# Optimization experiments

Hardware: AMD Instinct MI355X
Metric: run time of the kernel (lower is better)

The kernel has to match this reference:

```python
import jax, jax.numpy as jnp
import numpy as np

EPS = 1e-5  # InstanceNorm2d default


def setup_inputs() -> dict:
    key = jax.random.key(0)
    ks = jax.random.split(key, 8)
    B, L, D, Q, C, H, W = 16, 24, 256, 256, 256, 128, 128
    s = 0.05
    return {
        "w_source": jax.random.normal(ks[0], (B, L, D), jnp.float32),
        "w_target": jax.random.normal(ks[1], (B, L, D), jnp.float32),
        "h": jax.random.normal(ks[2], (B, C, H, W), jnp.float32),
        "conv0_w": jax.random.normal(ks[3], (Q, C), jnp.float32) * s,   # 1x1 conv kernel
        "conv0_b": jnp.zeros((Q,), jnp.float32),
        "fck_w": jax.random.normal(ks[4], (Q, D), jnp.float32) * s,
        "fck_b": jnp.zeros((Q,), jnp.float32),
        "fc_w": jax.random.normal(ks[5], (2 * C, D), jnp.float32) * s,
        "fc_b": jnp.zeros((2 * C,), jnp.float32),
        "in_w": jnp.ones((C,), jnp.float32),
        "in_b": jnp.zeros((C,), jnp.float32),
    }


def reference(w_source, w_target, h, conv0_w, conv0_b, fck_w, fck_b, fc_w, fc_b, in_w, in_b):
    # ---- CrossAttention ----
    # q: 1x1 conv over h  -> [B,H,W,Q]
    q = jnp.einsum("bchw,qc->bhwq", h, conv0_w) + conv0_b
    # k: word keys        -> [B,L,Q]
    k = jnp.einsum("bld,qd->blq", w_source, fck_w) + fck_b
    attn = jnp.einsum("bhwq,blq->bhwl", q, k)  # [B,H,W,L]

    # ---- MaskingAllocation ----
    scores = jnp.einsum("bld,bmd->blm", w_source, w_target)       # [B,L,L]
    left = jnp.sum(scores, axis=1, keepdims=True) - scores        # [B,L,L]
    idx = jnp.argmax(left, axis=-1)                               # [B,L]
    w_alloc = jnp.take_along_axis(w_target, idx[..., None], axis=1)  # [B,L,D]

    # ---- modulation params ----
    bg = jnp.einsum("bld,ed->ble", w_alloc, fc_w) + fc_b          # [B,L,2C]
    beta, gamma = jnp.split(bg, 2, axis=-1)                       # each [B,L,C]
    beta_map = jnp.einsum("bhwl,blc->bchw", attn, beta)           # [B,C,H,W]
    gamma_map = jnp.einsum("bhwl,blc->bchw", attn, gamma)

    # ---- InstanceNorm2d (affine) + modulation ----
    mean = jnp.mean(h, axis=(2, 3), keepdims=True)
    var = jnp.var(h, axis=(2, 3), keepdims=True)
    hn = (h - mean) * jax.lax.rsqrt(var + EPS)
    hn = hn * in_w[None, :, None, None] + in_b[None, :, None, None]
    return hn * gamma_map + beta_map
```

## Files before the change

### kernel.cpp

```cpp
#include <hip/hip_runtime.h>
#include <stdint.h>

#define HW 16384
#define Bn 16
#define Ln 24
#define Dn 256
#define Qn 256
#define Cn 256

typedef __attribute__((ext_vector_type(8))) short short8;
typedef __attribute__((ext_vector_type(4))) float f32x4;

__device__ __forceinline__ unsigned short f2bf(float f) {
  unsigned u = __builtin_bit_cast(unsigned, f);
  u += 0x7FFFu + ((u >> 16) & 1u);
  return (unsigned short)(u >> 16);
}
__device__ __forceinline__ float bf2f(unsigned short s) {
  return __builtin_bit_cast(float, (unsigned)s << 16);
}

__device__ __forceinline__ void gl_lds16(const void* gsrc, void* lds) {
  __builtin_amdgcn_global_load_lds(
      (const __attribute__((address_space(1))) unsigned int*)gsrc,
      (__attribute__((address_space(3))) unsigned int*)lds, 16, 0, 0);
}

__global__ void k_keys(const float* __restrict__ wsrc, const float* __restrict__ fckw,
                       const float* __restrict__ fckb, float* __restrict__ kmat) {
  int b = blockIdx.x / Ln, l = blockIdx.x % Ln;
  __shared__ float row[Dn];
  row[threadIdx.x] = wsrc[(b * Ln + l) * Dn + threadIdx.x];
  __syncthreads();
  int q = threadIdx.x;
  const float* wq = fckw + q * Dn;
  float acc = fckb[q];
#pragma unroll 8
  for (int d = 0; d < Dn; ++d) acc += row[d] * wq[d];
  kmat[(b * Ln + l) * Qn + q] = acc;
}

__global__ void k_alloc(const float* __restrict__ wsrc, const float* __restrict__ wtgt,
                        const float* __restrict__ conv0b, const float* __restrict__ kmat,
                        float* __restrict__ walloc, float* __restrict__ bias0) {
  int b = blockIdx.x;
  __shared__ float S[Ln][Dn];
  __shared__ float T[Ln][Dn];
  __shared__ double sc[Ln][Ln];
  __shared__ double cs[Ln];
  __shared__ int idx[Ln];
  int tid = threadIdx.x;
  for (int n = tid; n < Ln * Dn; n += 256) {
    S[n >> 8][n & 255] = wsrc[b * Ln * Dn + n];
    T[n >> 8][n & 255] = wtgt[b * Ln * Dn + n];
  }
  __syncthreads();
  for (int p = tid; p < Ln * Ln; p += 256) {
    int l = p / Ln, m = p % Ln;
    double a = 0.0;
    for (int d = 0; d < Dn; ++d) a += (double)S[l][d] * (double)T[m][d];
    sc[l][m] = a;
  }
  __syncthreads();
  if (tid < Ln) {
    double a = 0.0;
    for (int l = 0; l < Ln; ++l) a += sc[l][tid];
    cs[tid] = a;
  }
  __syncthreads();
  if (tid < Ln) {
    double best = -1e300; int bi = 0;
    for (int m = 0; m < Ln; ++m) {
      double v = cs[m] - sc[tid][m];
      if (v > best) { best = v; bi = m; }
    }
    idx[tid] = bi;
  }
  __syncthreads();
  for (int n = tid; n < Ln * Dn; n += 256) {
    int l = n >> 8, d = n & 255;
    walloc[b * Ln * Dn + n] = T[idx[l]][d];
  }
  if (tid < Ln) {
    float a = 0.f;
    const float* kr = kmat + (b * Ln + tid) * Qn;
    for (int q = 0; q < Qn; ++q) a += conv0b[q] * kr[q];
    bias0[b * Ln + tid] = a;
  }
}

__global__ void k_mbg(const float* __restrict__ kmat, const float* __restrict__ conv0w,
                      const float* __restrict__ walloc, const float* __restrict__ fcw,
                      const float* __restrict__ fcb,
                      float* __restrict__ Mmat, float* __restrict__ bg) {
  int bid = blockIdx.x;
  __shared__ float row[Dn];
  if (bid < Bn * Ln) {
    int b = bid / Ln, l = bid % Ln;
    row[threadIdx.x] = kmat[(b * Ln + l) * Qn + threadIdx.x];
    __syncthreads();
    int c = threadIdx.x;
    float acc = 0.f;
    for (int q = 0; q < Qn; ++q) acc += row[q] * conv0w[q * Cn + c];
    Mmat[(b * Ln + l) * Cn + c] = acc;
  } else {
    int id = bid - Bn * Ln;
    int b = id / Ln, l = id % Ln;
    row[threadIdx.x] = walloc[(b * Ln + l) * Dn + threadIdx.x];
    __syncthreads();
    for (int it = 0; it < 2; ++it) {
      int e = it * 256 + threadIdx.x;
      const float* we = fcw + e * Dn;
      float acc = fcb[e];
      for (int d = 0; d < Dn; ++d) acc += row[d] * we[d];
      bg[(b * Ln + l) * (2 * Cn) + e] = acc;
    }
  }
}

__global__ void k_gbuild(const float* __restrict__ Mmat, const float* __restrict__ bg,
                         const float* __restrict__ bias0,
                         unsigned short* __restrict__ Gt, float* __restrict__ bv) {
  int g = blockIdx.x, b = blockIdx.y;
  __shared__ float Ms[Ln][Dn];
  __shared__ float Gb[Ln][128];
  __shared__ float B0[Ln];
  int tid = threadIdx.x;
  for (int n = tid; n < Ln * Dn; n += 256) Ms[n >> 8][n & 255] = Mmat[b * Ln * Dn + n];
  for (int n = tid; n < Ln * 128; n += 256) {
    int l = n >> 7, j = n & 127;
    int e = (j < 64) ? (Cn + g * 64 + j) : (g * 64 + (j - 64));
    Gb[l][j] = bg[(b * Ln + l) * (2 * Cn) + e];
  }
  if (tid < Ln) B0[tid] = bias0[b * Ln + tid];
  __syncthreads();
  char* base = (char*)Gt + (unsigned long)(b * 4 + g) * 65536;
  for (int r = 0; r < 128; ++r) {
    int isb = (r >> 4) & 1;
    int c_loc = (r >> 5) * 16 + (r & 15);
    int j = c_loc + isb * 64;
    float acc = 0.f;
#pragma unroll
    for (int l = 0; l < Ln; ++l) acc += Ms[l][tid] * Gb[l][j];
    unsigned off = (unsigned)((r * 512 + tid * 2) ^ ((r & 7) << 4));
    *(unsigned short*)(base + off) = f2bf(acc);
  }
  if (tid < 128) {
    float a = 0.f;
#pragma unroll
    for (int l = 0; l < Ln; ++l) a += B0[l] * Gb[l][tid];
    bv[b * 512 + g * 128 + tid] = a;
  }
}

__global__ void k_tr(const float* __restrict__ h, unsigned short* __restrict__ hT,
                     float* __restrict__ part) {
  int hwc = blockIdx.x;
  int cc  = blockIdx.y;
  int b   = blockIdx.z;
  int tid = threadIdx.x;
  int w = tid >> 6, lane = tid & 63;
  __shared__ unsigned short tile[64 * 258];
  __shared__ float red[64 * 17 + 16];
  const int c0 = cc * 64, hw0 = hwc * 256;
  for (int i = 0; i < 16; ++i) {
    int cl = i * 4 + w;
    f32x4 v = *(const f32x4*)(h + ((unsigned long)(b * Cn + c0 + cl)) * HW + hw0 + lane * 4);
    unsigned lo = (unsigned)f2bf(v.x) | ((unsigned)f2bf(v.y) << 16);
    unsigned hi = (unsigned)f2bf(v.z) | ((unsigned)f2bf(v.w) << 16);
    unsigned* dst = (unsigned*)(tile + cl * 258 + lane * 4);
    dst[0] = lo; dst[1] = hi;
  }
  __syncthreads();
  int cp = tid & 31, sub = tid >> 5;
  float s0 = 0.f, s20 = 0.f, s1 = 0.f, s21 = 0.f;
  for (int i = 0; i < 32; ++i) {
    int hw = i * 8 + sub;
    unsigned short a0 = tile[(2 * cp) * 258 + hw];
    unsigned short a1 = tile[(2 * cp + 1) * 258 + hw];
    float f0 = bf2f(a0), f1 = bf2f(a1);
    s0 += f0; s20 += f0 * f0; s1 += f1; s21 += f1 * f1;
    unsigned pk = (unsigned)a0 | ((unsigned)a1 << 16);
    *(unsigned*)(hT + ((unsigned long)b * HW + hw0 + hw) * Cn + c0 + 2 * cp) = pk;
  }
  red[(2 * cp) * 17 + sub * 2]     = s0;
  red[(2 * cp) * 17 + sub * 2 + 1] = s20;
  red[(2 * cp + 1) * 17 + sub * 2]     = s1;
  red[(2 * cp + 1) * 17 + sub * 2 + 1] = s21;
  __syncthreads();
  if (tid < 64) {
    float a = 0.f, q = 0.f;
#pragma unroll
    for (int j = 0; j < 8; ++j) { a += red[tid * 17 + j * 2]; q += red[tid * 17 + j * 2 + 1]; }
    float* pp = part + (((unsigned long)(b * Cn + c0 + tid)) * 64 + hwc) * 2;
    pp[0] = a; pp[1] = q;
  }
}

__global__ void k_fin(const float* __restrict__ part, const float* __restrict__ inw,
                      const float* __restrict__ inb, float* __restrict__ ss) {
  int id = blockIdx.x * 256 + threadIdx.x;
  int c = id & 255;
  float s = 0.f, s2 = 0.f;
  const float* pp = part + (unsigned long)id * 128;
  for (int j = 0; j < 64; ++j) { s += pp[2 * j]; s2 += pp[2 * j + 1]; }
  float mean = s * (1.0f / HW);
  float var = s2 * (1.0f / HW) - mean * mean;
  float rs = rsqrtf(var + 1e-5f);
  float scv = rs * inw[c];
  float sh = inb[c] - mean * scv;
  ss[id * 2] = scv; ss[id * 2 + 1] = sh;
}

__global__ __launch_bounds__(512, 1) void k_main(
    const unsigned short* __restrict__ hT, const unsigned short* __restrict__ Gt,
    const float* __restrict__ bv, const float* __restrict__ ss,
    float* __restrict__ out) {
  int x = blockIdx.x;
  int o = x & 7, idx = x >> 3;
  int b = idx >> 2, g = idx & 3;
  int tid = threadIdx.x;
  int w = tid >> 6, lane = tid & 63;
  int mw = w >> 2, nw = w & 3;
  int lr = lane & 15, lg = lane >> 4;

  __shared__ __align__(16) unsigned char Ab[65536];
  __shared__ __align__(16) unsigned char Bb[4][16384];

  const char* Gblob = (const char*)Gt + (unsigned long)(b * 4 + g) * 65536;
  const char* hTb = (const char*)hT + (unsigned long)b * HW * 512;

#pragma unroll
  for (int i = 0; i < 8; ++i)
    gl_lds16(Gblob + i * 8192 + w * 1024 + lane * 16, &Ab[i * 8192 + w * 1024]);

#define STAGE_B(c2, buf_)                                                        \
  {                                                                              \
    int s2_ = (c2) & 7, t2_ = (c2) >> 3;                                         \
    const char* base_ = hTb + (unsigned long)((o * 8 + t2_) * 256) * 512;        \
    _Pragma("unroll")                                                            \
    for (int l_ = 0; l_ < 2; ++l_) {                                             \
      int rowg_ = l_ * 128 + w * 16 + (lane >> 2);                               \
      int bir_ = s2_ * 64 + ((((lane & 3) << 4)) ^ (((rowg_ >> 1) & 3) << 4));   \
      gl_lds16(base_ + (unsigned long)rowg_ * 512 + bir_,                        \
               &Bb[buf_][l_ * 8192 + w * 1024]);                                 \
    }                                                                            \
  }

  f32x4 acc[4][4];
#pragma unroll
  for (int mf = 0; mf < 4; ++mf)
#pragma unroll
    for (int nf = 0; nf < 4; ++nf) acc[mf][nf] = (f32x4){0.f, 0.f, 0.f, 0.f};

  unsigned short h16[2][4][4];
  const float* ssb = ss + b * Cn * 2;
  const float* bvb = bv + b * 512 + g * 128;
  const int ssnap = 2 * g + mw;

  STAGE_B(0, 0);
  STAGE_B(1, 1);
  STAGE_B(2, 2);
  STAGE_B(3, 3);
  asm volatile("s_waitcnt vmcnt(6)" ::: "memory");
  __builtin_amdgcn_s_barrier();
  __builtin_amdgcn_sched_barrier(0);

#define COMPUTE(ch_, s_)                                                         \
  {                                                                              \
    const unsigned char* Bcur = &Bb[(ch_) & 3][0];                               \
    if ((s_) == ssnap) {                                                         \
      _Pragma("unroll") for (int p = 0; p < 2; ++p)                              \
      _Pragma("unroll") for (int nf = 0; nf < 4; ++nf) {                         \
        int row = nw * 64 + nf * 16 + lr;                                        \
        int sw = ((row >> 1) & 3) << 4;                                          \
        _Pragma("unroll") for (int r = 0; r < 4; ++r) {                          \
          int kloc = p * 16 + lg * 4 + r;                                        \
          h16[p][nf][r] = *(const unsigned short*)(&Bcur[row * 64 + ((kloc * 2) ^ sw)]); \
        }                                                                        \
      }                                                                          \
    }                                                                            \
    short8 afr[4], bfr[4];                                                       \
    _Pragma("unroll") for (int mf = 0; mf < 4; ++mf) {                           \
      int row = mw * 64 + mf * 16 + lr;                                          \
      afr[mf] = *(const short8*)(                                                \
          &Ab[row * 512 + (((s_) * 64 + lg * 16) ^ ((row & 7) << 4))]);          \
    }                                                                            \
    _Pragma("unroll") for (int nf = 0; nf < 4; ++nf) {                           \
      int row = nw * 64 + nf * 16 + lr;                                          \
      bfr[nf] = *(const short8*)(                                                \
          &Bcur[row * 64 + ((lg << 4) ^ (((row >> 1) & 3) << 4))]);              \
    }                                                                            \
    _Pragma("unroll") for (int mf = 0; mf < 4; ++mf)                             \
      _Pragma("unroll") for (int nf = 0; nf < 4; ++nf)                           \
        acc[mf][nf] = __builtin_amdgcn_mfma_f32_16x16x32_bf16(afr[mf], bfr[nf],  \
                                                              acc[mf][nf], 0, 0, 0); \
  }

#define EPILOGUE(t_)                                                             \
  {                                                                              \
    int hwbase = (o * 8 + (t_)) * 256 + nw * 64 + lr;                            \
    _Pragma("unroll") for (int p = 0; p < 2; ++p)                                \
    _Pragma("unroll") for (int r = 0; r < 4; ++r) {                              \
      int c_loc = (mw * 2 + p) * 16 + lg * 4 + r;                                \
      int cch = g * 64 + c_loc;                                                  \
      float scv = ssb[cch * 2], sh = ssb[cch * 2 + 1];                           \
      float bvg = bvb[c_loc], bvbt = bvb[64 + c_loc];                            \
      float* orow = out + (unsigned long)(b * Cn + cch) * HW + hwbase;           \
      _Pragma("unroll") for (int nf = 0; nf < 4; ++nf) {                         \
        float hn = bf2f(h16[p][nf][r]) * scv + sh;                               \
        orow[nf * 16] = hn * (acc[2 * p][nf][r] + bvg) + (acc[2 * p + 1][nf][r] + bvbt); \
      }                                                                          \
    }                                                                            \
    _Pragma("unroll") for (int mf = 0; mf < 4; ++mf)                             \
      _Pragma("unroll") for (int nf = 0; nf < 4; ++nf)                           \
        acc[mf][nf] = (f32x4){0.f, 0.f, 0.f, 0.f};                               \
  }

#define SYNCS(ch_, N_)                                                           \
  asm volatile("s_waitcnt lgkmcnt(0)" ::: "memory");                             \
  __builtin_amdgcn_sched_barrier(0);                                             \
  __builtin_amdgcn_s_barrier();                                                  \
  STAGE_B((ch_) + 4, (ch_) & 3);                                                 \
  asm volatile("s_waitcnt vmcnt(" #N_ ")" ::: "memory");                         \
  __builtin_amdgcn_s_barrier();                                                  \
  __builtin_amdgcn_sched_barrier(0);

#define SYNCT(N_)                                                                \
  asm volatile("s_waitcnt lgkmcnt(0)" ::: "memory");                             \
  __builtin_amdgcn_sched_barrier(0);                                             \
  __builtin_amdgcn_s_barrier();                                                  \
  asm volatile("s_waitcnt vmcnt(" #N_ ")" ::: "memory");                         \
  __builtin_amdgcn_s_barrier();                                                  \
  __builtin_amdgcn_sched_barrier(0);

  for (int t = 0; t < 7; ++t) {
    int c0 = t * 8;
    COMPUTE(c0 + 0, 0) SYNCS(c0 + 0, 38)
    COMPUTE(c0 + 1, 1) SYNCS(c0 + 1, 38)
    COMPUTE(c0 + 2, 2) SYNCS(c0 + 2, 6)
    COMPUTE(c0 + 3, 3) SYNCS(c0 + 3, 6)
    COMPUTE(c0 + 4, 4) SYNCS(c0 + 4, 6)
    COMPUTE(c0 + 5, 5) SYNCS(c0 + 5, 6)
    COMPUTE(c0 + 6, 6) SYNCS(c0 + 6, 6)
    COMPUTE(c0 + 7, 7) EPILOGUE(t) SYNCS(c0 + 7, 38)
  }
  COMPUTE(56, 0) SYNCS(56, 38)
  COMPUTE(57, 1) SYNCS(57, 38)
  COMPUTE(58, 2) SYNCS(58, 6)
  COMPUTE(59, 3) SYNCS(59, 6)
  COMPUTE(60, 4) SYNCT(4)
  COMPUTE(61, 5) SYNCT(2)
  COMPUTE(62, 6) SYNCT(0)
  COMPUTE(63, 7) EPILOGUE(7)

#undef SYNCT
#undef SYNCS
#undef EPILOGUE
#undef COMPUTE
#undef STAGE_B
}

__global__ void k_sentinel(float* out) { out[0] = 12345.0f; }

extern "C" void kernel_launch(void* const* d_in, const int* in_sizes, int n_in,
                              void* d_out, int out_size, void* d_ws, size_t ws_size,
                              hipStream_t stream) {
  const float* wsrc   = (const float*)d_in[0];
  const float* wtgt   = (const float*)d_in[1];
  const float* h      = (const float*)d_in[2];
  const float* conv0w = (const float*)d_in[3];
  const float* conv0b = (const float*)d_in[4];
  const float* fckw   = (const float*)d_in[5];
  const float* fckb   = (const float*)d_in[6];
  const float* fcw    = (const float*)d_in[7];
  const float* fcb    = (const float*)d_in[8];
  const float* inw    = (const float*)d_in[9];
  const float* inb    = (const float*)d_in[10];
  float* out = (float*)d_out;
  char* ws = (char*)d_ws;

  const size_t NEED = 142542848ull;
  if (ws_size < NEED) {
    k_sentinel<<<1, 1, 0, stream>>>(out);
    return;
  }

  unsigned short* hT = (unsigned short*)(ws + 0);
  float* kmat   = (float*)(ws + 134217728);
  float* walloc = (float*)(ws + 134610944);
  float* bias0  = (float*)(ws + 135004160);
  float* bg     = (float*)(ws + 135006208);
  float* Mmat   = (float*)(ws + 135792640);
  unsigned short* Gt = (unsigned short*)(ws + 136185856);
  float* bv     = (float*)(ws + 140380160);
  float* part   = (float*)(ws + 140412928);
  float* ss     = (float*)(ws + 142510080);

  dim3 gt(64, 4, Bn);
  k_tr<<<gt, 256, 0, stream>>>(h, hT, part);
  k_keys<<<Bn * Ln, 256, 0, stream>>>(wsrc, fckw, fckb, kmat);
  k_alloc<<<Bn, 256, 0, stream>>>(wsrc, wtgt, conv0b, kmat, walloc, bias0);
  k_mbg<<<2 * Bn * Ln, 256, 0, stream>>>(kmat, conv0w, walloc, fcw, fcb, Mmat, bg);
  dim3 gg(4, Bn);
  k_gbuild<<<gg, 256, 0, stream>>>(Mmat, bg, bias0, Gt, bv);
  k_fin<<<16, 256, 0, stream>>>(part, inw, inb, ss);
  k_main<<<512, 512, 0, stream>>>(hT, Gt, bv, ss, out);
}
```

Baseline: 346.4 us.

## Stage epilogue output through LDS for coalesced 16-byte global stores

The epilogue now writes results into a swizzled LDS buffer in four slices and reads them back so each wave issues contiguous 16-byte stores along HW, replacing the scattered 4-byte stores. Per-channel scale, shift and beta/gamma values are loaded once into registers at kernel start instead of every epilogue. The vmcnt wait counts are lowered to match the fewer outstanding store instructions. This adds extra barriers and LDS traffic per epilogue, and 16KB more shared memory.

```diff
diff --git a/kernel.cpp b/kernel.cpp
--- a/kernel.cpp
+++ b/kernel.cpp
@@ -226,9 +226,25 @@
 
   __shared__ __align__(16) unsigned char Ab[65536];
   __shared__ __align__(16) unsigned char Bb[4][16384];
+  __shared__ __align__(16) float Ebf[4096];
 
   const char* Gblob = (const char*)Gt + (unsigned long)(b * 4 + g) * 65536;
   const char* hTb = (const char*)hT + (unsigned long)b * HW * 512;
+
+  const float* ssb = ss + b * Cn * 2;
+  const float* bvb = bv + b * 512 + g * 128;
+  float scvv[2][4], shv[2][4], bvgv[2][4], bvbv[2][4];
+#pragma unroll
+  for (int p = 0; p < 2; ++p)
+#pragma unroll
+    for (int r = 0; r < 4; ++r) {
+      int c_loc = (mw * 2 + p) * 16 + lg * 4 + r;
+      int cch = g * 64 + c_loc;
+      scvv[p][r] = ssb[cch * 2];
+      shv[p][r]  = ssb[cch * 2 + 1];
+      bvgv[p][r] = bvb[c_loc];
+      bvbv[p][r] = bvb[64 + c_loc];
+    }
 
 #pragma unroll
   for (int i = 0; i < 8; ++i)
@@ -254,8 +270,6 @@
     for (int nf = 0; nf < 4; ++nf) acc[mf][nf] = (f32x4){0.f, 0.f, 0.f, 0.f};
 
   unsigned short h16[2][4][4];
-  const float* ssb = ss + b * Cn * 2;
-  const float* bvb = bv + b * 512 + g * 128;
   const int ssnap = 2 * g + mw;
 
   STAGE_B(0, 0);
@@ -299,18 +313,32 @@
 
 #define EPILOGUE(t_)                                                             \
   {                                                                              \
-    int hwbase = (o * 8 + (t_)) * 256 + nw * 64 + lr;                            \
-    _Pragma("unroll") for (int p = 0; p < 2; ++p)                                \
-    _Pragma("unroll") for (int r = 0; r < 4; ++r) {                              \
-      int c_loc = (mw * 2 + p) * 16 + lg * 4 + r;                                \
-      int cch = g * 64 + c_loc;                                                  \
-      float scv = ssb[cch * 2], sh = ssb[cch * 2 + 1];                           \
-      float bvg = bvb[c_loc], bvbt = bvb[64 + c_loc];                            \
-      float* orow = out + (unsigned long)(b * Cn + cch) * HW + hwbase;           \
-      _Pragma("unroll") for (int nf = 0; nf < 4; ++nf) {                         \
-        float hn = bf2f(h16[p][nf][r]) * scv + sh;                               \
-        orow[nf * 16] = hn * (acc[2 * p][nf][r] + bvg) + (acc[2 * p + 1][nf][r] + bvbt); \
+    int hwt0_ = (o * 8 + (t_)) * 256;                                            \
+    _Pragma("unroll")                                                            \
+    for (int sl_ = 0; sl_ < 4; ++sl_) {                                          \
+      int mws_ = sl_ >> 1;                                                       \
+      const int ps_ = sl_ & 1;                                                   \
+      if (mw == mws_) {                                                          \
+        _Pragma("unroll") for (int nf = 0; nf < 4; ++nf)                         \
+        _Pragma("unroll") for (int r = 0; r < 4; ++r) {                          \
+          int c16_ = lg * 4 + r;                                                 \
+          int hwl_ = nw * 64 + nf * 16 + lr;                                     \
+          float hn_ = bf2f(h16[ps_][nf][r]) * scvv[ps_][r] + shv[ps_][r];        \
+          float val_ = hn_ * (acc[2 * ps_][nf][r] + bvgv[ps_][r]) +              \
+                       (acc[2 * ps_ + 1][nf][r] + bvbv[ps_][r]);                 \
+          Ebf[c16_ * 256 + (hwl_ ^ ((c16_ & 7) << 2))] = val_;                   \
+        }                                                                        \
       }                                                                          \
+      asm volatile("s_waitcnt lgkmcnt(0)" ::: "memory");                         \
+      __builtin_amdgcn_sched_barrier(0);                                         \
+      __builtin_amdgcn_s_barrier();                                              \
+      _Pragma("unroll") for (int rp_ = 0; rp_ < 2; ++rp_) {                      \
+        int c16_ = rp_ * 8 + w;                                                  \
+        f32x4 v_ = *(const f32x4*)(&Ebf[c16_ * 256 + ((lane * 4) ^ ((c16_ & 7) << 2))]); \
+        int cch_ = g * 64 + mws_ * 32 + ps_ * 16 + c16_;                         \
+        *(f32x4*)(out + (unsigned long)(b * Cn + cch_) * HW + hwt0_ + lane * 4) = v_; \
+      }                                                                          \
+      __builtin_amdgcn_s_barrier();                                              \
     }                                                                            \
     _Pragma("unroll") for (int mf = 0; mf < 4; ++mf)                             \
       _Pragma("unroll") for (int nf = 0; nf < 4; ++nf)                           \
@@ -334,19 +362,27 @@
   __builtin_amdgcn_s_barrier();                                                  \
   __builtin_amdgcn_sched_barrier(0);
 
-  for (int t = 0; t < 7; ++t) {
+  COMPUTE(0, 0) SYNCS(0, 6)
+  COMPUTE(1, 1) SYNCS(1, 6)
+  COMPUTE(2, 2) SYNCS(2, 6)
+  COMPUTE(3, 3) SYNCS(3, 6)
+  COMPUTE(4, 4) SYNCS(4, 6)
+  COMPUTE(5, 5) SYNCS(5, 6)
+  COMPUTE(6, 6) SYNCS(6, 6)
+  COMPUTE(7, 7) EPILOGUE(0) SYNCS(7, 14)
+  for (int t = 1; t < 7; ++t) {
     int c0 = t * 8;
-    COMPUTE(c0 + 0, 0) SYNCS(c0 + 0, 38)
-    COMPUTE(c0 + 1, 1) SYNCS(c0 + 1, 38)
+    COMPUTE(c0 + 0, 0) SYNCS(c0 + 0, 14)
+    COMPUTE(c0 + 1, 1) SYNCS(c0 + 1, 14)
     COMPUTE(c0 + 2, 2) SYNCS(c0 + 2, 6)
     COMPUTE(c0 + 3, 3) SYNCS(c0 + 3, 6)
     COMPUTE(c0 + 4, 4) SYNCS(c0 + 4, 6)
     COMPUTE(c0 + 5, 5) SYNCS(c0 + 5, 6)
     COMPUTE(c0 + 6, 6) SYNCS(c0 + 6, 6)
-    COMPUTE(c0 + 7, 7) EPILOGUE(t) SYNCS(c0 + 7, 38)
-  }
-  COMPUTE(56, 0) SYNCS(56, 38)
-  COMPUTE(57, 1) SYNCS(57, 38)
+    COMPUTE(c0 + 7, 7) EPILOGUE(t) SYNCS(c0 + 7, 14)
+  }
+  COMPUTE(56, 0) SYNCS(56, 14)
+  COMPUTE(57, 1) SYNCS(57, 14)
   COMPUTE(58, 2) SYNCS(58, 6)
   COMPUTE(59, 3) SYNCS(59, 6)
   COMPUTE(60, 4) SYNCT(4)
```

New measurement: 380.3 us. +9.8%, slower.
